# Performance work log

Hardware: AMD Instinct MI355X
Metric: run time of the kernel (lower is better)

Reference implementation:

```python
import jax, jax.numpy as jnp
import numpy as np

EPS = 1e-12  # torch F.normalize default eps


def setup_inputs() -> dict:
    key = jax.random.key(0)
    k1, k2, k3 = jax.random.split(key, 3)
    ns, d_in, n_feat, n_classes = 16384, 512, 256, 1000
    x = jax.random.normal(k1, (ns, d_in), dtype=jnp.float32)
    W = jax.random.normal(k2, (d_in, n_feat), dtype=jnp.float32) * 0.05
    # class prototypes: L2-normalized embeddings, one per seen class (seen_c == n_classes)
    means = jax.random.normal(k3, (n_classes, n_feat), dtype=jnp.float32)
    means = means / jnp.maximum(jnp.linalg.norm(means, axis=1, keepdims=True), EPS)
    return {"x": x, "W": W, "means": means, "t": 0}


def reference(x, W, means, t):
    # forward_training: backbone + L2 normalization along feature dim
    feats = x @ W                                   # [ns, n_feat]
    preds = feats / jnp.maximum(jnp.linalg.norm(feats, axis=1, keepdims=True), EPS)
    # deployment forward: nearest prototype by negative dot product
    # original: per-sample dist = -means @ pred^T; dist.min(0) -> class index
    dist = -(preds @ means.T)                       # [ns, seen_c]
    classpred = jnp.argmin(dist, axis=1)            # first min on ties, matches torch
    n_classes = means.shape[0]
    out = jax.nn.one_hot(classpred, n_classes, dtype=jnp.float32)  # [ns, n_classes]
    return out
```

## Files before the change

kernel.cpp:

```cpp
#include <hip/hip_runtime.h>
#include <float.h>

#define NS   16384
#define K1   512
#define F    256
#define NC   1000
#define SPB  32
#define NTHR 512
#define NBLK (NS / SPB)


typedef _Float16 half8 __attribute__((ext_vector_type(8)));
typedef float    float4v __attribute__((ext_vector_type(4)));

#define WH_OFF 0
#define WL_OFF 131072
#define MH_OFF 262144
#define ML_OFF (262144 + 262144)

__global__ void prep_w(const float* __restrict__ W, _Float16* __restrict__ ws) {
    int g    = blockIdx.x * blockDim.x + threadIdx.x;
    int lane = g & 63, tile = g >> 6;
    int ks = tile >> 4, nt = tile & 15;
    int k0 = ks * 32 + (lane >> 4) * 8;
    int n  = nt * 16 + (lane & 15);
    _Float16 h[8], l[8];
#pragma unroll
    for (int j = 0; j < 8; ++j) {
        float v = W[(size_t)(k0 + j) * F + n] * 16.0f;
        _Float16 hi = (_Float16)v;
        h[j] = hi;
        l[j] = (_Float16)(v - (float)hi);
    }
    _Float16* dh = ws + WH_OFF + (size_t)g * 8;
    _Float16* dl = ws + WL_OFF + (size_t)g * 8;
#pragma unroll
    for (int j = 0; j < 8; ++j) { dh[j] = h[j]; dl[j] = l[j]; }
}

__global__ void prep_m(const float* __restrict__ means, _Float16* __restrict__ ws) {
    int g    = blockIdx.x * blockDim.x + threadIdx.x;
    int lane = g & 63, tile = g >> 6;
    int ks = tile >> 6, gt = tile & 63;
    int k0 = ks * 32 + (lane >> 4) * 8;
    int c  = gt * 16 + (lane & 15);
    _Float16 h[8], l[8];
#pragma unroll
    for (int j = 0; j < 8; ++j) {
        float v = (c < NC) ? means[(size_t)c * F + k0 + j] * 16.0f : 0.0f;
        _Float16 hi = (_Float16)v;
        h[j] = hi;
        l[j] = (_Float16)(v - (float)hi);
    }
    _Float16* dh = ws + MH_OFF + (size_t)g * 8;
    _Float16* dl = ws + ML_OFF + (size_t)g * 8;
#pragma unroll
    for (int j = 0; j < 8; ++j) { dh[j] = h[j]; dl[j] = l[j]; }
}

#define MFMA(a, b, c) __builtin_amdgcn_mfma_f32_16x16x32_f16((a), (b), (c), 0, 0, 0)

__attribute__((amdgpu_flat_work_group_size(NTHR, NTHR), amdgpu_waves_per_eu(2, 4)))
__global__ void fused_mfma(const float* __restrict__ x,
                           const _Float16* __restrict__ ws,
                           float* __restrict__ out) {
    __shared__ _Float16 xsh[2][32][44];
    __shared__ _Float16 xsl[2][32][44];
    __shared__ _Float16 fh[32][264];
    __shared__ _Float16 fl[32][264];
    __shared__ float cand_v[32][8];
    __shared__ int   cand_i[32][8];
    __shared__ int   bidx[32];

    const int tid  = threadIdx.x;
    const int lane = tid & 63;
    const int w    = tid >> 6;
    const int quad = lane >> 4;
    const int cl   = lane & 15;
    const int s0   = blockIdx.x * SPB;

    const int xrow = tid >> 4;
    const int xc   = (tid & 15) * 2;

    float4v acc1[2][2];
#pragma unroll
    for (int p = 0; p < 2; ++p)
#pragma unroll
        for (int mt = 0; mt < 2; ++mt)
            acc1[p][mt] = (float4v){0.f, 0.f, 0.f, 0.f};

    float2 xv = *reinterpret_cast<const float2*>(x + (size_t)(s0 + xrow) * K1 + xc);

    for (int ks = 0; ks < 16; ++ks) {
        const int buf = ks & 1;
        {
            float vx = xv.x * 8.0f, vy = xv.y * 8.0f;
            _Float16 hx = (_Float16)vx, hy = (_Float16)vy;
            xsh[buf][xrow][xc]     = hx;
            xsh[buf][xrow][xc + 1] = hy;
            xsl[buf][xrow][xc]     = (_Float16)(vx - (float)hx);
            xsl[buf][xrow][xc + 1] = (_Float16)(vy - (float)hy);
        }
        __syncthreads();
        if (ks < 15)
            xv = *reinterpret_cast<const float2*>(
                x + (size_t)(s0 + xrow) * K1 + (ks + 1) * 32 + xc);

        half8 ah[2], al[2];
#pragma unroll
        for (int mt = 0; mt < 2; ++mt) {
            ah[mt] = *reinterpret_cast<const half8*>(&xsh[buf][mt * 16 + cl][quad * 8]);
            al[mt] = *reinterpret_cast<const half8*>(&xsl[buf][mt * 16 + cl][quad * 8]);
        }
#pragma unroll
        for (int p = 0; p < 2; ++p) {
            const int tile = ks * 16 + (w * 2 + p);
            half8 bh = *reinterpret_cast<const half8*>(
                ws + WH_OFF + ((size_t)tile * 64 + lane) * 8);
            half8 bl = *reinterpret_cast<const half8*>(
                ws + WL_OFF + ((size_t)tile * 64 + lane) * 8);
#pragma unroll
            for (int mt = 0; mt < 2; ++mt) {
                acc1[p][mt] = MFMA(ah[mt], bh, acc1[p][mt]);
                acc1[p][mt] = MFMA(ah[mt], bl, acc1[p][mt]);
                acc1[p][mt] = MFMA(al[mt], bh, acc1[p][mt]);
            }
        }
    }

#pragma unroll
    for (int p = 0; p < 2; ++p)
#pragma unroll
        for (int mt = 0; mt < 2; ++mt)
#pragma unroll
            for (int r = 0; r < 4; ++r) {
                int srow = mt * 16 + quad * 4 + r;
                int n    = (w * 2 + p) * 16 + cl;
                float v  = acc1[p][mt][r];
                _Float16 hi = (_Float16)v;
                fh[srow][n] = hi;
                fl[srow][n] = (_Float16)(v - (float)hi);
            }
    __syncthreads();

    float4v acc2[2][8];
#pragma unroll
    for (int mt = 0; mt < 2; ++mt)
#pragma unroll
        for (int nt = 0; nt < 8; ++nt)
            acc2[mt][nt] = (float4v){0.f, 0.f, 0.f, 0.f};

    for (int ks = 0; ks < 8; ++ks) {
        half8 fah[2], fal[2];
#pragma unroll
        for (int mt = 0; mt < 2; ++mt) {
            fah[mt] = *reinterpret_cast<const half8*>(
                &fh[mt * 16 + cl][ks * 32 + quad * 8]);
            fal[mt] = *reinterpret_cast<const half8*>(
                &fl[mt * 16 + cl][ks * 32 + quad * 8]);
        }
#pragma unroll
        for (int nt = 0; nt < 8; ++nt) {
            const int tile = ks * 64 + (w * 8 + nt);
            half8 mh = *reinterpret_cast<const half8*>(
                ws + MH_OFF + ((size_t)tile * 64 + lane) * 8);
            half8 ml = *reinterpret_cast<const half8*>(
                ws + ML_OFF + ((size_t)tile * 64 + lane) * 8);
#pragma unroll
            for (int mt = 0; mt < 2; ++mt) {
                acc2[mt][nt] = MFMA(fah[mt], mh, acc2[mt][nt]);
                acc2[mt][nt] = MFMA(fah[mt], ml, acc2[mt][nt]);
                acc2[mt][nt] = MFMA(fal[mt], mh, acc2[mt][nt]);
            }
        }
    }

#pragma unroll
    for (int mt = 0; mt < 2; ++mt)
#pragma unroll
        for (int r = 0; r < 4; ++r) {
            float v  = -FLT_MAX;
            int   ix = 0x7FFFFFFF;
#pragma unroll
            for (int nt = 0; nt < 8; ++nt) {
                int c = (w * 8 + nt) * 16 + cl;
                if (c < NC) {
                    float sc = acc2[mt][nt][r];
                    if (sc > v) { v = sc; ix = c; }
                }
            }
#pragma unroll
            for (int off = 1; off < 16; off <<= 1) {
                float ov = __shfl_xor(v, off, 64);
                int   oi = __shfl_xor(ix, off, 64);
                if (ov > v || (ov == v && oi < ix)) { v = ov; ix = oi; }
            }
            if (cl == 0) {
                int srow = mt * 16 + quad * 4 + r;
                cand_v[srow][w] = v;
                cand_i[srow][w] = ix;
            }
        }
    __syncthreads();

    if (tid < 32) {
        float v  = cand_v[tid][0];
        int   ix = cand_i[tid][0];
#pragma unroll
        for (int q = 1; q < 8; ++q) {
            float ov = cand_v[tid][q];
            int   oi = cand_i[tid][q];
            if (ov > v || (ov == v && oi < ix)) { v = ov; ix = oi; }
        }
        bidx[tid] = ix;
    }
    __syncthreads();

    const int NF4 = NC / 4;
    for (int q = tid; q < SPB * NF4; q += NTHR) {
        int row   = q / NF4;
        int c4    = q - row * NF4;
        int b     = bidx[row];
        int cbase = c4 * 4;
        float4 v;
        v.x = (cbase + 0 == b) ? 1.f : 0.f;
        v.y = (cbase + 1 == b) ? 1.f : 0.f;
        v.z = (cbase + 2 == b) ? 1.f : 0.f;
        v.w = (cbase + 3 == b) ? 1.f : 0.f;
        *reinterpret_cast<float4*>(out + (size_t)(s0 + row) * NC + cbase) = v;
    }
}

extern "C" void kernel_launch(void* const* d_in, const int* in_sizes, int n_in,
                              void* d_out, int out_size, void* d_ws, size_t ws_size,
                              hipStream_t stream) {
    const float* x     = (const float*)d_in[0];
    const float* W     = (const float*)d_in[1];
    const float* means = (const float*)d_in[2];
    float* out         = (float*)d_out;
    _Float16* ws       = (_Float16*)d_ws;

    prep_w<<<64, 256, 0, stream>>>(W, ws);
    prep_m<<<128, 256, 0, stream>>>(means, ws);
    fused_mfma<<<NBLK, NTHR, 0, stream>>>(x, ws, out);
}
```

Baseline: 138.1 us.

## Prefetch weight/prototype fragments into registers, interleave hi/lo layout, merge prep kernels

Result: no change. 140.2 us (+1.5%).

```diff
diff --git a/kernel.cpp b/kernel.cpp
--- a/kernel.cpp
+++ b/kernel.cpp
@@ -10,52 +10,49 @@
 #define NBLK (NS / SPB)
 
 
-typedef _Float16 half8 __attribute__((ext_vector_type(8)));
+typedef _Float16 half8  __attribute__((ext_vector_type(8)));
 typedef float    float4v __attribute__((ext_vector_type(4)));
-
-#define WH_OFF 0
-#define WL_OFF 131072
-#define MH_OFF 262144
-#define ML_OFF (262144 + 262144)
-
-__global__ void prep_w(const float* __restrict__ W, _Float16* __restrict__ ws) {
-    int g    = blockIdx.x * blockDim.x + threadIdx.x;
-    int lane = g & 63, tile = g >> 6;
-    int ks = tile >> 4, nt = tile & 15;
-    int k0 = ks * 32 + (lane >> 4) * 8;
-    int n  = nt * 16 + (lane & 15);
-    _Float16 h[8], l[8];
-#pragma unroll
-    for (int j = 0; j < 8; ++j) {
-        float v = W[(size_t)(k0 + j) * F + n] * 16.0f;
-        _Float16 hi = (_Float16)v;
-        h[j] = hi;
-        l[j] = (_Float16)(v - (float)hi);
-    }
-    _Float16* dh = ws + WH_OFF + (size_t)g * 8;
-    _Float16* dl = ws + WL_OFF + (size_t)g * 8;
-#pragma unroll
-    for (int j = 0; j < 8; ++j) { dh[j] = h[j]; dl[j] = l[j]; }
-}
-
-__global__ void prep_m(const float* __restrict__ means, _Float16* __restrict__ ws) {
-    int g    = blockIdx.x * blockDim.x + threadIdx.x;
-    int lane = g & 63, tile = g >> 6;
-    int ks = tile >> 6, gt = tile & 63;
-    int k0 = ks * 32 + (lane >> 4) * 8;
-    int c  = gt * 16 + (lane & 15);
-    _Float16 h[8], l[8];
-#pragma unroll
-    for (int j = 0; j < 8; ++j) {
-        float v = (c < NC) ? means[(size_t)c * F + k0 + j] * 16.0f : 0.0f;
-        _Float16 hi = (_Float16)v;
-        h[j] = hi;
-        l[j] = (_Float16)(v - (float)hi);
-    }
-    _Float16* dh = ws + MH_OFF + (size_t)g * 8;
-    _Float16* dl = ws + ML_OFF + (size_t)g * 8;
-#pragma unroll
-    for (int j = 0; j < 8; ++j) { dh[j] = h[j]; dl[j] = l[j]; }
+typedef float    float2v __attribute__((ext_vector_type(2)));
+
+#define M_OFF 262144
+
+__global__ void prep(const float* __restrict__ W, const float* __restrict__ means,
+                     _Float16* __restrict__ ws) {
+    int g = blockIdx.x * blockDim.x + threadIdx.x;
+    if (g < 16384) {
+        int lane = g & 63, tile = g >> 6;
+        int ks = tile >> 4, nt = tile & 15;
+        int k0 = ks * 32 + (lane >> 4) * 8;
+        int n  = nt * 16 + (lane & 15);
+        half8 hv, lv;
+#pragma unroll
+        for (int j = 0; j < 8; ++j) {
+            float v = W[(size_t)(k0 + j) * F + n] * 16.0f;
+            _Float16 hi = (_Float16)v;
+            hv[j] = hi;
+            lv[j] = (_Float16)(v - (float)hi);
+        }
+        _Float16* d = ws + (size_t)tile * 1024 + (size_t)lane * 8;
+        *reinterpret_cast<half8*>(d)       = hv;
+        *reinterpret_cast<half8*>(d + 512) = lv;
+    } else {
+        int gm = g - 16384;
+        int lane = gm & 63, tile = gm >> 6;
+        int ks = tile >> 6, gt = tile & 63;
+        int k0 = ks * 32 + (lane >> 4) * 8;
+        int c  = gt * 16 + (lane & 15);
+        half8 hv, lv;
+#pragma unroll
+        for (int j = 0; j < 8; ++j) {
+            float v = (c < NC) ? means[(size_t)c * F + k0 + j] * 16.0f : 0.0f;
+            _Float16 hi = (_Float16)v;
+            hv[j] = hi;
+            lv[j] = (_Float16)(v - (float)hi);
+        }
+        _Float16* d = ws + M_OFF + (size_t)tile * 1024 + (size_t)lane * 8;
+        *reinterpret_cast<half8*>(d)       = hv;
+        *reinterpret_cast<half8*>(d + 512) = lv;
+    }
 }
 
 #define MFMA(a, b, c) __builtin_amdgcn_mfma_f32_16x16x32_f16((a), (b), (c), 0, 0, 0)
@@ -89,8 +86,18 @@
         for (int mt = 0; mt < 2; ++mt)
             acc1[p][mt] = (float4v){0.f, 0.f, 0.f, 0.f};
 
-    float2 xv = *reinterpret_cast<const float2*>(x + (size_t)(s0 + xrow) * K1 + xc);
-
+    const _Float16* wsrc = ws + ((size_t)(w * 2) << 10) + ((size_t)lane << 3);
+    half8 wbh[2][2], wbl[2][2];
+#pragma unroll
+    for (int p = 0; p < 2; ++p) {
+        wbh[0][p] = *reinterpret_cast<const half8*>(wsrc + p * 1024);
+        wbl[0][p] = *reinterpret_cast<const half8*>(wsrc + p * 1024 + 512);
+    }
+
+    float2v xv = __builtin_nontemporal_load(
+        reinterpret_cast<const float2v*>(x + (size_t)(s0 + xrow) * K1 + xc));
+
+#pragma unroll
     for (int ks = 0; ks < 16; ++ks) {
         const int buf = ks & 1;
         {
@@ -101,11 +108,20 @@
             xsl[buf][xrow][xc]     = (_Float16)(vx - (float)hx);
             xsl[buf][xrow][xc + 1] = (_Float16)(vy - (float)hy);
         }
+        if (ks < 15)
+            xv = __builtin_nontemporal_load(
+                reinterpret_cast<const float2v*>(
+                    x + (size_t)(s0 + xrow) * K1 + (ks + 1) * 32 + xc));
         __syncthreads();
-        if (ks < 15)
-            xv = *reinterpret_cast<const float2*>(
-                x + (size_t)(s0 + xrow) * K1 + (ks + 1) * 32 + xc);
-
+        if (ks < 15) {
+#pragma unroll
+            for (int p = 0; p < 2; ++p) {
+                wbh[buf ^ 1][p] = *reinterpret_cast<const half8*>(
+                    wsrc + (size_t)(ks + 1) * 16384 + p * 1024);
+                wbl[buf ^ 1][p] = *reinterpret_cast<const half8*>(
+                    wsrc + (size_t)(ks + 1) * 16384 + p * 1024 + 512);
+            }
+        }
         half8 ah[2], al[2];
 #pragma unroll
         for (int mt = 0; mt < 2; ++mt) {
@@ -113,19 +129,13 @@
             al[mt] = *reinterpret_cast<const half8*>(&xsl[buf][mt * 16 + cl][quad * 8]);
         }
 #pragma unroll
-        for (int p = 0; p < 2; ++p) {
-            const int tile = ks * 16 + (w * 2 + p);
-            half8 bh = *reinterpret_cast<const half8*>(
-                ws + WH_OFF + ((size_t)tile * 64 + lane) * 8);
-            half8 bl = *reinterpret_cast<const half8*>(
-                ws + WL_OFF + ((size_t)tile * 64 + lane) * 8);
+        for (int p = 0; p < 2; ++p)
 #pragma unroll
             for (int mt = 0; mt < 2; ++mt) {
-                acc1[p][mt] = MFMA(ah[mt], bh, acc1[p][mt]);
-                acc1[p][mt] = MFMA(ah[mt], bl, acc1[p][mt]);
-                acc1[p][mt] = MFMA(al[mt], bh, acc1[p][mt]);
-            }
-        }
+                acc1[p][mt] = MFMA(ah[mt], wbh[buf][p], acc1[p][mt]);
+                acc1[p][mt] = MFMA(ah[mt], wbl[buf][p], acc1[p][mt]);
+                acc1[p][mt] = MFMA(al[mt], wbh[buf][p], acc1[p][mt]);
+            }
     }
 
 #pragma unroll
@@ -150,27 +160,54 @@
         for (int nt = 0; nt < 8; ++nt)
             acc2[mt][nt] = (float4v){0.f, 0.f, 0.f, 0.f};
 
-    for (int ks = 0; ks < 8; ++ks) {
-        half8 fah[2], fal[2];
-#pragma unroll
-        for (int mt = 0; mt < 2; ++mt) {
-            fah[mt] = *reinterpret_cast<const half8*>(
-                &fh[mt * 16 + cl][ks * 32 + quad * 8]);
-            fal[mt] = *reinterpret_cast<const half8*>(
-                &fl[mt * 16 + cl][ks * 32 + quad * 8]);
-        }
-#pragma unroll
-        for (int nt = 0; nt < 8; ++nt) {
-            const int tile = ks * 64 + (w * 8 + nt);
-            half8 mh = *reinterpret_cast<const half8*>(
-                ws + MH_OFF + ((size_t)tile * 64 + lane) * 8);
-            half8 ml = *reinterpret_cast<const half8*>(
-                ws + ML_OFF + ((size_t)tile * 64 + lane) * 8);
+    const _Float16* mbase = ws + M_OFF + ((size_t)(w * 8) << 10) + ((size_t)lane << 3);
+
+    half8 mh[2][2], ml[2][2];
+    half8 fah[2][2], fal[2][2];
+#pragma unroll
+    for (int t = 0; t < 2; ++t) {
+        mh[0][t] = *reinterpret_cast<const half8*>(mbase + t * 1024);
+        ml[0][t] = *reinterpret_cast<const half8*>(mbase + t * 1024 + 512);
+    }
+#pragma unroll
+    for (int mt = 0; mt < 2; ++mt) {
+        fah[0][mt] = *reinterpret_cast<const half8*>(&fh[mt * 16 + cl][quad * 8]);
+        fal[0][mt] = *reinterpret_cast<const half8*>(&fl[mt * 16 + cl][quad * 8]);
+    }
+
+#pragma unroll
+    for (int b = 0; b < 32; ++b) {
+        const int cb = b & 1;
+        const int ks = b >> 2;
+        const int ab = ks & 1;
+        if (b < 31) {
+            const int b2 = b + 1;
+            const _Float16* src =
+                mbase + (size_t)((b2 >> 2) * 65536 + (b2 & 3) * 2048);
+#pragma unroll
+            for (int t = 0; t < 2; ++t) {
+                mh[cb ^ 1][t] = *reinterpret_cast<const half8*>(src + t * 1024);
+                ml[cb ^ 1][t] = *reinterpret_cast<const half8*>(src + t * 1024 + 512);
+            }
+        }
+        if ((b & 3) == 2 && ks < 7) {
 #pragma unroll
             for (int mt = 0; mt < 2; ++mt) {
-                acc2[mt][nt] = MFMA(fah[mt], mh, acc2[mt][nt]);
-                acc2[mt][nt] = MFMA(fah[mt], ml, acc2[mt][nt]);
-                acc2[mt][nt] = MFMA(fal[mt], mh, acc2[mt][nt]);
+                fah[ab ^ 1][mt] = *reinterpret_cast<const half8*>(
+                    &fh[mt * 16 + cl][(ks + 1) * 32 + quad * 8]);
+                fal[ab ^ 1][mt] = *reinterpret_cast<const half8*>(
+                    &fl[mt * 16 + cl][(ks + 1) * 32 + quad * 8]);
+            }
+        }
+        const int n0 = (b & 3) * 2;
+#pragma unroll
+        for (int t = 0; t < 2; ++t) {
+            const int nt = n0 + t;
+#pragma unroll
+            for (int mt = 0; mt < 2; ++mt) {
+                acc2[mt][nt] = MFMA(fah[ab][mt], mh[cb][t], acc2[mt][nt]);
+                acc2[mt][nt] = MFMA(fah[ab][mt], ml[cb][t], acc2[mt][nt]);
+                acc2[mt][nt] = MFMA(fal[ab][mt], mh[cb][t], acc2[mt][nt]);
             }
         }
     }
@@ -222,12 +259,13 @@
         int c4    = q - row * NF4;
         int b     = bidx[row];
         int cbase = c4 * 4;
-        float4 v;
+        float4v v;
         v.x = (cbase + 0 == b) ? 1.f : 0.f;
         v.y = (cbase + 1 == b) ? 1.f : 0.f;
         v.z = (cbase + 2 == b) ? 1.f : 0.f;
         v.w = (cbase + 3 == b) ? 1.f : 0.f;
-        *reinterpret_cast<float4*>(out + (size_t)(s0 + row) * NC + cbase) = v;
+        __builtin_nontemporal_store(
+            v, reinterpret_cast<float4v*>(out + (size_t)(s0 + row) * NC + cbase));
     }
 }
 
@@ -240,7 +278,6 @@
     float* out         = (float*)d_out;
     _Float16* ws       = (_Float16*)d_ws;
 
-    prep_w<<<64, 256, 0, stream>>>(W, ws);
-    prep_m<<<128, 256, 0, stream>>>(means, ws);
+    prep<<<192, 256, 0, stream>>>(W, means, ws);
     fused_mfma<<<NBLK, NTHR, 0, stream>>>(x, ws, out);
 }
```
